# Performance work log

Hardware: AMD Instinct MI355X
Metric: run time of the kernel (lower is better)

## Reference

```python
import jax, jax.numpy as jnp
import numpy as np
import math

K_SLOTS = 64
DIM = 512
HEADS = 8
HEAD_DIM = DIM // HEADS
EPS = 1e-20
LN_EPS = 1e-5
SQRT_DIM = 1.0 / math.sqrt(HEAD_DIM)


def layernorm(x, g, b):
    mu = jnp.mean(x, axis=-1, keepdims=True)
    var = jnp.var(x, axis=-1, keepdims=True)
    return (x - mu) * jax.lax.rsqrt(var + LN_EPS) * g + b


def setup_inputs() -> dict:
    key = jax.random.key(0)
    ks = jax.random.split(key, 8)
    B, T = 8, 8192
    lim = 1.0 / math.sqrt(DIM)
    return {
        "X": jax.random.normal(ks[0], (B, T, DIM), jnp.float32),
        "slots_w": jax.random.normal(ks[1], (K_SLOTS, DIM), jnp.float32),
        "g_slots": jnp.ones((DIM,), jnp.float32),
        "b_slots": jnp.zeros((DIM,), jnp.float32),
        "Wk": jax.random.uniform(ks[2], (DIM, DIM), jnp.float32, -lim, lim),
        "bk": jax.random.uniform(ks[3], (DIM,), jnp.float32, -lim, lim),
        "Wv": jax.random.uniform(ks[4], (DIM, DIM), jnp.float32, -lim, lim),
        "bv": jax.random.uniform(ks[5], (DIM,), jnp.float32, -lim, lim),
        "g_after": jnp.ones((DIM,), jnp.float32),
        "b_after": jnp.zeros((DIM,), jnp.float32),
    }


def reference(X, slots_w, g_slots, b_slots, Wk, bk, Wv, bv, g_after, b_after):
    B, T, D = X.shape
    # slots -> queries, shared across batch: (K, D) -> (H, K, hd)
    S = layernorm(slots_w, g_slots, b_slots)
    Q = S.reshape(K_SLOTS, HEADS, HEAD_DIM).transpose(1, 0, 2)  # (H, K, hd)
    # key/value projections, head split: (B, T, D) -> (B, H, T, hd)
    Kx = (X @ Wk.T + bk).reshape(B, T, HEADS, HEAD_DIM).transpose(0, 2, 1, 3)
    V = (X @ Wv.T + bv).reshape(B, T, HEADS, HEAD_DIM).transpose(0, 2, 1, 3)
    # attention logits (B, H, K, T), scale = 1/sqrt(head_dim)
    A = jnp.einsum("hkd,bhsd->bhks", Q, Kx) * SQRT_DIM
    # softmax over the SLOT axis (k), then renormalize by row-sum over s
    W = jax.nn.softmax(A, axis=-2)
    C = jnp.sum(W, axis=-1, keepdims=True)  # (B, H, K, 1)
    A = W / (C + EPS)
    S_hat = jnp.einsum("bhks,bhsd->bhkd", A, V)  # (B, H, K, hd)
    S_hat = S_hat.transpose(0, 2, 1, 3).reshape(B, K_SLOTS, D)
    return layernorm(S_hat, g_after, b_after)
```

## Files before the change

### kernel.cpp

```cpp
#include <hip/hip_runtime.h>
#include <hip/hip_bf16.h>
#include <math.h>

typedef unsigned short ushort_t;
typedef unsigned int u32;

constexpr int D  = 512;
constexpr int T  = 8192;
constexpr int B  = 8;
constexpr int H  = 8;
constexpr int KS = 64;
constexpr int HD = 64;
constexpr float SCALE = 0.125f;
constexpr float LNEPS = 1e-5f;
constexpr float EPS   = 1e-20f;

constexpr int TC  = 128;
constexpr int CPB = 2;

constexpr size_t OFF_S    = 0;
constexpr size_t OFF_BQ   = 32768;
constexpr size_t OFF_SACC = 33280;
constexpr size_t OFF_CACC = 295424;
constexpr size_t OFF_WB2  = 299520;

typedef __attribute__((ext_vector_type(8))) short bf16x8;
typedef __attribute__((ext_vector_type(4))) float f32x4;
typedef __attribute__((ext_vector_type(4))) unsigned short us4;

typedef const __attribute__((address_space(1))) u32* gas_ptr;
typedef __attribute__((address_space(3))) u32* las_ptr;

__device__ __forceinline__ void gload16(const void* g, void* l) {
  __builtin_amdgcn_global_load_lds((gas_ptr)g, (las_ptr)l, 16, 0, 0);
}

__device__ __forceinline__ ushort_t f2bf(float x) {
  __hip_bfloat16 t = __float2bfloat16(x);
  return *(ushort_t*)&t;
}

__device__ __forceinline__ u32 pk2bf(float x, float y) {
  __hip_bfloat162 t = __float22bfloat162_rn(make_float2(x, y));
  return *(u32*)&t;
}

__device__ __forceinline__ bf16x8 cvt8(f32x4 a, f32x4 b) {
  union { bf16x8 v; u32 u[4]; } r;
  r.u[0] = pk2bf(a.x, a.y); r.u[1] = pk2bf(a.z, a.w);
  r.u[2] = pk2bf(b.x, b.y); r.u[3] = pk2bf(b.z, b.w);
  return r.v;
}

__global__ void ln_slots_kernel(const float* __restrict__ slots_w,
                                const float* __restrict__ g, const float* __restrict__ b,
                                float* __restrict__ S) {
  __shared__ float red[8];
  int k = blockIdx.x;
  int tid = threadIdx.x;
  float x0 = slots_w[k*D + tid];
  float x1 = slots_w[k*D + tid + 256];
  float s1 = x0 + x1, s2 = x0*x0 + x1*x1;
  for (int off = 32; off; off >>= 1) { s1 += __shfl_xor(s1, off); s2 += __shfl_xor(s2, off); }
  if ((tid & 63) == 0) { red[tid >> 6] = s1; red[4 + (tid >> 6)] = s2; }
  __syncthreads();
  s1 = red[0] + red[1] + red[2] + red[3];
  s2 = red[4] + red[5] + red[6] + red[7];
  float mu = s1 / D;
  float var = s2 / D - mu * mu;
  float rs = rsqrtf(var + LNEPS);
  S[k*D + tid]       = (x0 - mu) * rs * g[tid]       + b[tid];
  S[k*D + tid + 256] = (x1 - mu) * rs * g[tid + 256] + b[tid + 256];
}

__global__ void weff_kernel(const float* __restrict__ S, const float* __restrict__ Wk,
                            ushort_t* __restrict__ Wb2) {
  int gid = blockIdx.x * 256 + threadIdx.x;
  int in = gid & 511;
  int hk = gid >> 9;
  int h = hk >> 6, k = hk & 63;
  const float* srow = S + k*D + h*HD;
  const float* wcol = Wk + (size_t)(h*HD)*D + in;
  float acc = 0.f;
  #pragma unroll 8
  for (int d = 0; d < HD; ++d) acc += srow[d] * wcol[(size_t)d*D];
  Wb2[(size_t)(h*128 + k)*D + in] = f2bf(acc * SCALE);
}

__global__ void bq_kernel(const float* __restrict__ S, const float* __restrict__ bk,
                          float* __restrict__ bq) {
  int hk = blockIdx.x * 256 + threadIdx.x;
  int h = hk >> 6, k = hk & 63;
  float acc = 0.f;
  for (int d = 0; d < HD; ++d) acc += S[k*D + h*HD + d] * bk[h*HD + d];
  bq[hk] = acc * SCALE;
}

__global__ void wvcopy_kernel(const float* __restrict__ Wv, ushort_t* __restrict__ Wb2) {
  int gid = blockIdx.x * 256 + threadIdx.x;
  int in = gid & 511;
  int hd = gid >> 9;
  int h = hd >> 6, d = hd & 63;
  Wb2[(size_t)(h*128 + 64 + d)*D + in] = f2bf(Wv[(size_t)hd*D + in]);
}

__global__ void zero_kernel(float* __restrict__ p, int n) {
  int gid = blockIdx.x * 256 + threadIdx.x;
  if (gid < n) p[gid] = 0.f;
}

__global__ __launch_bounds__(256, 3) void main_kernel(
    const float* __restrict__ X, const ushort_t* __restrict__ Wb2,
    const float* __restrict__ bq, const float* __restrict__ bv,
    float* __restrict__ Sacc, float* __restrict__ Cacc) {
  __shared__ __align__(16) char smem[34816];
  float*    A_lds = (float*)smem;
  ushort_t* B_lds = (ushort_t*)(smem + 16384);
  ushort_t* W_lds = (ushort_t*)smem;
  ushort_t* V_lds = (ushort_t*)(smem + 17408);

  const int tid  = threadIdx.x;
  const int lane = tid & 63, w = tid >> 6;
  const int wm = w & 1, wn = w >> 1;
  const int m16 = lane & 15, q = lane >> 4;

  const int id = blockIdx.x;
  const int h  = (id >> 3) & 7;
  const int cg = (id & 7) | ((id >> 6) << 3);
  const int bh = (cg >> 5) * H + h;

  f32x4 acc2[4] = {};
  float csum[4] = {0.f, 0.f, 0.f, 0.f};

  for (int cc = 0; cc < CPB; ++cc) {
    const float* Xc = X + (size_t)(cg * CPB + cc) * TC * D;
    f32x4 acc[4][4] = {};

    for (int kb = 0; kb < D; kb += 32) {
      __syncthreads();
      #pragma unroll
      for (int m = 0; m < 4; ++m) {
        int li = tid + m * 256;
        int row = li >> 3, c = li & 7;
        gload16(Xc + (size_t)row * D + kb + c * 4, A_lds + (size_t)li * 4);
      }
      #pragma unroll
      for (int m = 0; m < 2; ++m) {
        int li = tid + m * 256;
        int col = li >> 2, c = li & 3;
        gload16(Wb2 + (size_t)(h * 128 + col) * D + kb + c * 8, B_lds + (size_t)li * 8);
      }
      __syncthreads();
      bf16x8 af[4], bf[4];
      #pragma unroll
      for (int i = 0; i < 4; ++i) {
        const f32x4* ap = (const f32x4*)(A_lds + (wm * 64 + i * 16 + m16) * 32 + q * 8);
        af[i] = cvt8(ap[0], ap[1]);
      }
      #pragma unroll
      for (int j = 0; j < 4; ++j)
        bf[j] = *(const bf16x8*)(B_lds + (wn * 64 + j * 16 + m16) * 32 + q * 8);
      #pragma unroll
      for (int i = 0; i < 4; ++i)
        #pragma unroll
        for (int j = 0; j < 4; ++j)
          acc[i][j] = __builtin_amdgcn_mfma_f32_16x16x32_bf16(af[i], bf[j], acc[i][j], 0, 0, 0);
    }
    __syncthreads();

    if (wn == 0) {
      float bqv[4];
      #pragma unroll
      for (int j = 0; j < 4; ++j) bqv[j] = bq[h * KS + j * 16 + m16];
      #pragma unroll
      for (int i = 0; i < 4; ++i) {
        us4 wp[4];
        #pragma unroll
        for (int r = 0; r < 4; ++r) {
          float v0 = acc[i][0][r] + bqv[0];
          float v1 = acc[i][1][r] + bqv[1];
          float v2 = acc[i][2][r] + bqv[2];
          float v3 = acc[i][3][r] + bqv[3];
          float mx = fmaxf(fmaxf(v0, v1), fmaxf(v2, v3));
          mx = fmaxf(mx, __shfl_xor(mx, 1));
          mx = fmaxf(mx, __shfl_xor(mx, 2));
          mx = fmaxf(mx, __shfl_xor(mx, 4));
          mx = fmaxf(mx, __shfl_xor(mx, 8));
          v0 = __expf(v0 - mx); v1 = __expf(v1 - mx);
          v2 = __expf(v2 - mx); v3 = __expf(v3 - mx);
          float s = v0 + v1 + v2 + v3;
          s += __shfl_xor(s, 1); s += __shfl_xor(s, 2);
          s += __shfl_xor(s, 4); s += __shfl_xor(s, 8);
          float inv = __builtin_amdgcn_rcpf(s);
          v0 *= inv; v1 *= inv; v2 *= inv; v3 *= inv;
          csum[0] += v0; csum[1] += v1; csum[2] += v2; csum[3] += v3;
          wp[0][r] = f2bf(v0); wp[1][r] = f2bf(v1);
          wp[2][r] = f2bf(v2); wp[3][r] = f2bf(v3);
        }
        #pragma unroll
        for (int j = 0; j < 4; ++j)
          *(us4*)(W_lds + (j * 16 + m16) * 136 + wm * 64 + i * 16 + q * 4) = wp[j];
      }
    } else {
      float bvv[4];
      #pragma unroll
      for (int j = 0; j < 4; ++j) bvv[j] = bv[h * HD + j * 16 + m16];
      #pragma unroll
      for (int i = 0; i < 4; ++i) {
        #pragma unroll
        for (int j = 0; j < 4; ++j) {
          us4 pk;
          pk.x = f2bf(acc[i][j][0] + bvv[j]);
          pk.y = f2bf(acc[i][j][1] + bvv[j]);
          pk.z = f2bf(acc[i][j][2] + bvv[j]);
          pk.w = f2bf(acc[i][j][3] + bvv[j]);
          *(us4*)(V_lds + (j * 16 + m16) * 136 + wm * 64 + i * 16 + q * 4) = pk;
        }
      }
    }
    __syncthreads();

    #pragma unroll
    for (int kk = 0; kk < 4; ++kk) {
      bf16x8 a = *(const bf16x8*)(W_lds + (w * 16 + m16) * 136 + kk * 32 + q * 8);
      #pragma unroll
      for (int j = 0; j < 4; ++j) {
        bf16x8 bb = *(const bf16x8*)(V_lds + (j * 16 + m16) * 136 + kk * 32 + q * 8);
        acc2[j] = __builtin_amdgcn_mfma_f32_16x16x32_bf16(a, bb, acc2[j], 0, 0, 0);
      }
    }
  }

  float* Sb = Sacc + (size_t)bh * KS * HD;
  #pragma unroll
  for (int j = 0; j < 4; ++j)
    #pragma unroll
    for (int r = 0; r < 4; ++r)
      atomicAdd(Sb + (w * 16 + q * 4 + r) * HD + j * 16 + m16, acc2[j][r]);

  if (wn == 0) {
    #pragma unroll
    for (int j = 0; j < 4; ++j) {
      float c = csum[j];
      c += __shfl_xor(c, 16);
      c += __shfl_xor(c, 32);
      if (q == 0) atomicAdd(Cacc + (size_t)bh * KS + j * 16 + m16, c);
    }
  }
}

__global__ void finalize_kernel(const float* __restrict__ Sacc, const float* __restrict__ Cacc,
                                const float* __restrict__ g, const float* __restrict__ bb,
                                float* __restrict__ out) {
  __shared__ float red[8];
  int bk_ = blockIdx.x;
  int b = bk_ >> 6, k = bk_ & 63;
  int tid = threadIdx.x;
  float v[2];
  #pragma unroll
  for (int m = 0; m < 2; ++m) {
    int d = tid + m*256;
    int h = d >> 6, dd = d & 63;
    float c = Cacc[((size_t)b*H + h)*KS + k];
    v[m] = Sacc[(((size_t)b*H + h)*KS + k)*HD + dd] / (c + EPS);
  }
  float s1 = v[0] + v[1], s2 = v[0]*v[0] + v[1]*v[1];
  for (int off = 32; off; off >>= 1) { s1 += __shfl_xor(s1, off); s2 += __shfl_xor(s2, off); }
  if ((tid & 63) == 0) { red[tid >> 6] = s1; red[4 + (tid >> 6)] = s2; }
  __syncthreads();
  s1 = red[0] + red[1] + red[2] + red[3];
  s2 = red[4] + red[5] + red[6] + red[7];
  float mu = s1 / D;
  float var = s2 / D - mu * mu;
  float rs = rsqrtf(var + LNEPS);
  #pragma unroll
  for (int m = 0; m < 2; ++m) {
    int d = tid + m*256;
    out[(size_t)bk_*D + d] = (v[m] - mu) * rs * g[d] + bb[d];
  }
}

extern "C" void kernel_launch(void* const* d_in, const int* in_sizes, int n_in,
                              void* d_out, int out_size, void* d_ws, size_t ws_size,
                              hipStream_t stream) {
  const float* X       = (const float*)d_in[0];
  const float* slots_w = (const float*)d_in[1];
  const float* g_slots = (const float*)d_in[2];
  const float* b_slots = (const float*)d_in[3];
  const float* Wk      = (const float*)d_in[4];
  const float* bk      = (const float*)d_in[5];
  const float* Wv      = (const float*)d_in[6];
  const float* bv      = (const float*)d_in[7];
  const float* g_after = (const float*)d_in[8];
  const float* b_after = (const float*)d_in[9];
  float* ws   = (float*)d_ws;
  float* S    = ws + OFF_S;
  float* bq   = ws + OFF_BQ;
  float* Sacc = ws + OFF_SACC;
  float* Cacc = ws + OFF_CACC;
  ushort_t* Wb2 = (ushort_t*)(ws + OFF_WB2);
  float* out  = (float*)d_out;

  hipLaunchKernelGGL(ln_slots_kernel, dim3(64), dim3(256), 0, stream, slots_w, g_slots, b_slots, S);
  hipLaunchKernelGGL(weff_kernel, dim3(1024), dim3(256), 0, stream, S, Wk, Wb2);
  hipLaunchKernelGGL(bq_kernel, dim3(2), dim3(256), 0, stream, S, bk, bq);
  hipLaunchKernelGGL(wvcopy_kernel, dim3(1024), dim3(256), 0, stream, Wv, Wb2);
  hipLaunchKernelGGL(zero_kernel, dim3(1040), dim3(256), 0, stream, Sacc, 266240);
  hipLaunchKernelGGL(main_kernel, dim3(2048), dim3(256), 0, stream, X, Wb2, bq, bv, Sacc, Cacc);
  hipLaunchKernelGGL(finalize_kernel, dim3(B * KS), dim3(256), 0, stream,
                     Sacc, Cacc, g_after, b_after, out);
}
```

Before: 362.6 us.

## Double-buffer LDS tiles in the projection GEMM and swizzle LDS layout

The K-loop of the fused key/value projection now double-buffers the X and weight tiles in LDS. The next 32-wide slice is issued with direct global-to-LDS loads before computing on the current one, and explicit vmcnt waits plus raw barriers replace the two __syncthreads per iteration. It also applies an XOR swizzle to the LDS layout to reduce bank conflicts on fragment reads. LDS use grows from 34 KB to 48 KB per block, which may lower occupancy below the 3-blocks launch bound, and a trailing sync is added after the slot GEMM.

```diff
diff --git a/kernel.cpp b/kernel.cpp
--- a/kernel.cpp
+++ b/kernel.cpp
@@ -113,9 +113,11 @@
     const float* __restrict__ X, const ushort_t* __restrict__ Wb2,
     const float* __restrict__ bq, const float* __restrict__ bv,
     float* __restrict__ Sacc, float* __restrict__ Cacc) {
-  __shared__ __align__(16) char smem[34816];
-  float*    A_lds = (float*)smem;
-  ushort_t* B_lds = (ushort_t*)(smem + 16384);
+  __shared__ __align__(16) char smem[49152];
+  float*    A0 = (float*)smem;
+  float*    A1 = (float*)(smem + 16384);
+  ushort_t* B0 = (ushort_t*)(smem + 32768);
+  ushort_t* B1 = (ushort_t*)(smem + 40960);
   ushort_t* W_lds = (ushort_t*)smem;
   ushort_t* V_lds = (ushort_t*)(smem + 17408);
 
@@ -129,6 +131,8 @@
   const int cg = (id & 7) | ((id >> 6) << 3);
   const int bh = (cg >> 5) * H + h;
 
+  const ushort_t* Wp = Wb2 + (size_t)h * 128 * D;
+
   f32x4 acc2[4] = {};
   float csum[4] = {0.f, 0.f, 0.f, 0.f};
 
@@ -136,35 +140,70 @@
     const float* Xc = X + (size_t)(cg * CPB + cc) * TC * D;
     f32x4 acc[4][4] = {};
 
-    for (int kb = 0; kb < D; kb += 32) {
-      __syncthreads();
-      #pragma unroll
-      for (int m = 0; m < 4; ++m) {
-        int li = tid + m * 256;
-        int row = li >> 3, c = li & 7;
-        gload16(Xc + (size_t)row * D + kb + c * 4, A_lds + (size_t)li * 4);
-      }
-      #pragma unroll
-      for (int m = 0; m < 2; ++m) {
-        int li = tid + m * 256;
-        int col = li >> 2, c = li & 3;
-        gload16(Wb2 + (size_t)(h * 128 + col) * D + kb + c * 8, B_lds + (size_t)li * 8);
-      }
-      __syncthreads();
-      bf16x8 af[4], bf[4];
+    #pragma unroll
+    for (int m = 0; m < 4; ++m) {
+      int li = tid + m * 256;
+      int row = li >> 3, c = li & 7;
+      gload16(Xc + (size_t)row * D + ((c ^ (row & 7)) * 4), A0 + (size_t)li * 4);
+    }
+    #pragma unroll
+    for (int m = 0; m < 2; ++m) {
+      int li = tid + m * 256;
+      int col = li >> 2, c = li & 3;
+      gload16(Wp + (size_t)col * D + ((c ^ ((col >> 1) & 3)) * 8), B0 + (size_t)li * 8);
+    }
+
+    #pragma unroll 2
+    for (int t = 0; t < 16; ++t) {
+      const float*    Ab = (t & 1) ? A1 : A0;
+      const ushort_t* Bb = (t & 1) ? B1 : B0;
+      if (t < 15) {
+        float*    An = (t & 1) ? A0 : A1;
+        ushort_t* Bn = (t & 1) ? B0 : B1;
+        int kb = (t + 1) * 32;
+        #pragma unroll
+        for (int m = 0; m < 4; ++m) {
+          int li = tid + m * 256;
+          int row = li >> 3, c = li & 7;
+          gload16(Xc + (size_t)row * D + kb + ((c ^ (row & 7)) * 4), An + (size_t)li * 4);
+        }
+        #pragma unroll
+        for (int m = 0; m < 2; ++m) {
+          int li = tid + m * 256;
+          int col = li >> 2, c = li & 3;
+          gload16(Wp + (size_t)col * D + kb + ((c ^ ((col >> 1) & 3)) * 8), Bn + (size_t)li * 8);
+        }
+        asm volatile("s_waitcnt vmcnt(6)" ::: "memory");
+      } else {
+        asm volatile("s_waitcnt vmcnt(0)" ::: "memory");
+      }
+      __builtin_amdgcn_s_barrier();
+      __builtin_amdgcn_sched_barrier(0);
+
+      bf16x8 af[4], bfr[4];
       #pragma unroll
       for (int i = 0; i < 4; ++i) {
-        const f32x4* ap = (const f32x4*)(A_lds + (wm * 64 + i * 16 + m16) * 32 + q * 8);
-        af[i] = cvt8(ap[0], ap[1]);
-      }
-      #pragma unroll
-      for (int j = 0; j < 4; ++j)
-        bf[j] = *(const bf16x8*)(B_lds + (wn * 64 + j * 16 + m16) * 32 + q * 8);
+        int r = wm * 64 + i * 16 + m16;
+        int sw = r & 7;
+        f32x4 a0 = *(const f32x4*)(Ab + (size_t)r * 32 + (((2 * q)     ^ sw) * 4));
+        f32x4 a1 = *(const f32x4*)(Ab + (size_t)r * 32 + (((2 * q + 1) ^ sw) * 4));
+        af[i] = cvt8(a0, a1);
+      }
+      #pragma unroll
+      for (int j = 0; j < 4; ++j) {
+        int cl = wn * 64 + j * 16 + m16;
+        bfr[j] = *(const bf16x8*)(Bb + (size_t)cl * 32 + ((q ^ ((cl >> 1) & 3)) * 8));
+      }
       #pragma unroll
       for (int i = 0; i < 4; ++i)
         #pragma unroll
         for (int j = 0; j < 4; ++j)
-          acc[i][j] = __builtin_amdgcn_mfma_f32_16x16x32_bf16(af[i], bf[j], acc[i][j], 0, 0, 0);
+          acc[i][j] = __builtin_amdgcn_mfma_f32_16x16x32_bf16(af[i], bfr[j], acc[i][j], 0, 0, 0);
+
+      if (t < 15) {
+        __builtin_amdgcn_sched_barrier(0);
+        __builtin_amdgcn_s_barrier();
+      }
     }
     __syncthreads();
 
@@ -229,6 +268,7 @@
         acc2[j] = __builtin_amdgcn_mfma_f32_16x16x32_bf16(a, bb, acc2[j], 0, 0, 0);
       }
     }
+    __syncthreads();
   }
 
   float* Sb = Sacc + (size_t)bh * KS * HD;
```

Measured after the change: 359.9 us. About the same (-0.7%).

## Load GEMM operands directly from global into registers with double buffering

Applied to the files above, without the earlier changes.

Replaces the LDS-staged global_load_lds tiling of the projection GEMM with per-lane direct global loads into registers, software-pipelined over two K-steps. This removes the two barriers per K-step and the LDS round trip. The cost is higher register use (launch bounds drop to 2 waves per SIMD) and loss of cross-wave operand sharing, since each X row is now fetched by both wn waves and each weight row by both wm waves. A barrier is added at the end of each chunk to protect the reused LDS buffers.

```diff
diff --git a/kernel.cpp b/kernel.cpp
--- a/kernel.cpp
+++ b/kernel.cpp
@@ -27,13 +27,6 @@
 typedef __attribute__((ext_vector_type(8))) short bf16x8;
 typedef __attribute__((ext_vector_type(4))) float f32x4;
 typedef __attribute__((ext_vector_type(4))) unsigned short us4;
-
-typedef const __attribute__((address_space(1))) u32* gas_ptr;
-typedef __attribute__((address_space(3))) u32* las_ptr;
-
-__device__ __forceinline__ void gload16(const void* g, void* l) {
-  __builtin_amdgcn_global_load_lds((gas_ptr)g, (las_ptr)l, 16, 0, 0);
-}
 
 __device__ __forceinline__ ushort_t f2bf(float x) {
   __hip_bfloat16 t = __float2bfloat16(x);
@@ -109,13 +102,11 @@
   if (gid < n) p[gid] = 0.f;
 }
 
-__global__ __launch_bounds__(256, 3) void main_kernel(
+__global__ __launch_bounds__(256, 2) void main_kernel(
     const float* __restrict__ X, const ushort_t* __restrict__ Wb2,
     const float* __restrict__ bq, const float* __restrict__ bv,
     float* __restrict__ Sacc, float* __restrict__ Cacc) {
   __shared__ __align__(16) char smem[34816];
-  float*    A_lds = (float*)smem;
-  ushort_t* B_lds = (ushort_t*)(smem + 16384);
   ushort_t* W_lds = (ushort_t*)smem;
   ushort_t* V_lds = (ushort_t*)(smem + 17408);
 
@@ -129,44 +120,78 @@
   const int cg = (id & 7) | ((id >> 6) << 3);
   const int bh = (cg >> 5) * H + h;
 
+  const ushort_t* bp[4];
+  #pragma unroll
+  for (int j = 0; j < 4; ++j)
+    bp[j] = Wb2 + (size_t)(h * 128 + wn * 64 + j * 16 + m16) * D + q * 8;
+
   f32x4 acc2[4] = {};
   float csum[4] = {0.f, 0.f, 0.f, 0.f};
 
   for (int cc = 0; cc < CPB; ++cc) {
     const float* Xc = X + (size_t)(cg * CPB + cc) * TC * D;
+    const float* ap[4];
+    #pragma unroll
+    for (int i = 0; i < 4; ++i)
+      ap[i] = Xc + (size_t)(wm * 64 + i * 16 + m16) * D + q * 8;
+
     f32x4 acc[4][4] = {};
 
-    for (int kb = 0; kb < D; kb += 32) {
-      __syncthreads();
-      #pragma unroll
-      for (int m = 0; m < 4; ++m) {
-        int li = tid + m * 256;
-        int row = li >> 3, c = li & 7;
-        gload16(Xc + (size_t)row * D + kb + c * 4, A_lds + (size_t)li * 4);
-      }
-      #pragma unroll
-      for (int m = 0; m < 2; ++m) {
-        int li = tid + m * 256;
-        int col = li >> 2, c = li & 3;
-        gload16(Wb2 + (size_t)(h * 128 + col) * D + kb + c * 8, B_lds + (size_t)li * 8);
-      }
-      __syncthreads();
-      bf16x8 af[4], bf[4];
+    f32x4 aL0[4], aH0[4], aL1[4], aH1[4];
+    bf16x8 bF0[4], bF1[4];
+
+    #pragma unroll
+    for (int i = 0; i < 4; ++i) {
+      aL0[i] = *(const f32x4*)(ap[i]);
+      aH0[i] = *(const f32x4*)(ap[i] + 4);
+    }
+    #pragma unroll
+    for (int j = 0; j < 4; ++j) bF0[j] = *(const bf16x8*)(bp[j]);
+
+    #pragma unroll
+    for (int tt = 0; tt < 8; ++tt) {
+      const int t1 = 2 * tt + 1;
       #pragma unroll
       for (int i = 0; i < 4; ++i) {
-        const f32x4* ap = (const f32x4*)(A_lds + (wm * 64 + i * 16 + m16) * 32 + q * 8);
-        af[i] = cvt8(ap[0], ap[1]);
-      }
-      #pragma unroll
-      for (int j = 0; j < 4; ++j)
-        bf[j] = *(const bf16x8*)(B_lds + (wn * 64 + j * 16 + m16) * 32 + q * 8);
-      #pragma unroll
-      for (int i = 0; i < 4; ++i)
-        #pragma unroll
-        for (int j = 0; j < 4; ++j)
-          acc[i][j] = __builtin_amdgcn_mfma_f32_16x16x32_bf16(af[i], bf[j], acc[i][j], 0, 0, 0);
-    }
-    __syncthreads();
+        aL1[i] = *(const f32x4*)(ap[i] + t1 * 32);
+        aH1[i] = *(const f32x4*)(ap[i] + t1 * 32 + 4);
+      }
+      #pragma unroll
+      for (int j = 0; j < 4; ++j) bF1[j] = *(const bf16x8*)(bp[j] + t1 * 32);
+
+      {
+        bf16x8 af[4];
+        #pragma unroll
+        for (int i = 0; i < 4; ++i) af[i] = cvt8(aL0[i], aH0[i]);
+        #pragma unroll
+        for (int i = 0; i < 4; ++i)
+          #pragma unroll
+          for (int j = 0; j < 4; ++j)
+            acc[i][j] = __builtin_amdgcn_mfma_f32_16x16x32_bf16(af[i], bF0[j], acc[i][j], 0, 0, 0);
+      }
+
+      if (tt < 7) {
+        const int t2 = 2 * tt + 2;
+        #pragma unroll
+        for (int i = 0; i < 4; ++i) {
+          aL0[i] = *(const f32x4*)(ap[i] + t2 * 32);
+          aH0[i] = *(const f32x4*)(ap[i] + t2 * 32 + 4);
+        }
+        #pragma unroll
+        for (int j = 0; j < 4; ++j) bF0[j] = *(const bf16x8*)(bp[j] + t2 * 32);
+      }
+
+      {
+        bf16x8 af[4];
+        #pragma unroll
+        for (int i = 0; i < 4; ++i) af[i] = cvt8(aL1[i], aH1[i]);
+        #pragma unroll
+        for (int i = 0; i < 4; ++i)
+          #pragma unroll
+          for (int j = 0; j < 4; ++j)
+            acc[i][j] = __builtin_amdgcn_mfma_f32_16x16x32_bf16(af[i], bF1[j], acc[i][j], 0, 0, 0);
+      }
+    }
 
     if (wn == 0) {
       float bqv[4];
@@ -229,6 +254,7 @@
         acc2[j] = __builtin_amdgcn_mfma_f32_16x16x32_bf16(a, bb, acc2[j], 0, 0, 0);
       }
     }
+    __syncthreads();
   }
 
   float* Sb = Sacc + (size_t)bh * KS * HD;
```

New measurement: 785.4 us. 2.17x slower.

## Double-buffer X tiles with swizzled LDS, load B directly, merge setup kernels

Applied to the files above, without the earlier changes.

The main GEMM loop now double-buffers the X tile in LDS, prefetching the next K-step with async loads while the current one computes. Manual vmcnt waits and barriers replace the two __syncthreads per step. The A tile uses an XOR swizzle to cut LDS bank conflicts, and the Wb2 fragments are read straight from global memory into registers rather than staged through LDS. The setup kernels (bq, weff, wvcopy, zero) are folded into ln_slots and one combined setup kernel to save launches, at the cost of more registers and tight asm ordering that may lower occupancy.

```diff
diff --git a/kernel.cpp b/kernel.cpp
--- a/kernel.cpp
+++ b/kernel.cpp
@@ -54,7 +54,8 @@
 
 __global__ void ln_slots_kernel(const float* __restrict__ slots_w,
                                 const float* __restrict__ g, const float* __restrict__ b,
-                                float* __restrict__ S) {
+                                const float* __restrict__ bk,
+                                float* __restrict__ S, float* __restrict__ bq) {
   __shared__ float red[8];
   int k = blockIdx.x;
   int tid = threadIdx.x;
@@ -69,44 +70,46 @@
   float mu = s1 / D;
   float var = s2 / D - mu * mu;
   float rs = rsqrtf(var + LNEPS);
-  S[k*D + tid]       = (x0 - mu) * rs * g[tid]       + b[tid];
-  S[k*D + tid + 256] = (x1 - mu) * rs * g[tid + 256] + b[tid + 256];
-}
-
-__global__ void weff_kernel(const float* __restrict__ S, const float* __restrict__ Wk,
-                            ushort_t* __restrict__ Wb2) {
-  int gid = blockIdx.x * 256 + threadIdx.x;
-  int in = gid & 511;
-  int hk = gid >> 9;
-  int h = hk >> 6, k = hk & 63;
-  const float* srow = S + k*D + h*HD;
-  const float* wcol = Wk + (size_t)(h*HD)*D + in;
-  float acc = 0.f;
-  #pragma unroll 8
-  for (int d = 0; d < HD; ++d) acc += srow[d] * wcol[(size_t)d*D];
-  Wb2[(size_t)(h*128 + k)*D + in] = f2bf(acc * SCALE);
-}
-
-__global__ void bq_kernel(const float* __restrict__ S, const float* __restrict__ bk,
-                          float* __restrict__ bq) {
-  int hk = blockIdx.x * 256 + threadIdx.x;
-  int h = hk >> 6, k = hk & 63;
-  float acc = 0.f;
-  for (int d = 0; d < HD; ++d) acc += S[k*D + h*HD + d] * bk[h*HD + d];
-  bq[hk] = acc * SCALE;
-}
-
-__global__ void wvcopy_kernel(const float* __restrict__ Wv, ushort_t* __restrict__ Wb2) {
-  int gid = blockIdx.x * 256 + threadIdx.x;
-  int in = gid & 511;
-  int hd = gid >> 9;
-  int h = hd >> 6, d = hd & 63;
-  Wb2[(size_t)(h*128 + 64 + d)*D + in] = f2bf(Wv[(size_t)hd*D + in]);
-}
-
-__global__ void zero_kernel(float* __restrict__ p, int n) {
-  int gid = blockIdx.x * 256 + threadIdx.x;
-  if (gid < n) p[gid] = 0.f;
+  float y0 = (x0 - mu) * rs * g[tid]       + b[tid];
+  float y1 = (x1 - mu) * rs * g[tid + 256] + b[tid + 256];
+  S[k*D + tid]       = y0;
+  S[k*D + tid + 256] = y1;
+  float p0 = y0 * bk[tid];
+  float p1 = y1 * bk[tid + 256];
+  for (int off = 32; off; off >>= 1) { p0 += __shfl_xor(p0, off); p1 += __shfl_xor(p1, off); }
+  if ((tid & 63) == 0) {
+    int w = tid >> 6;
+    bq[w * KS + k]       = p0 * SCALE;
+    bq[(4 + w) * KS + k] = p1 * SCALE;
+  }
+}
+
+__global__ void setup_kernel(const float* __restrict__ S, const float* __restrict__ Wk,
+                             const float* __restrict__ Wv,
+                             ushort_t* __restrict__ Wb2, float* __restrict__ Sacc) {
+  int id = blockIdx.x;
+  int tid = threadIdx.x;
+  if (id < 1024) {
+    int gid = id * 256 + tid;
+    int in = gid & 511;
+    int hk = gid >> 9;
+    int h = hk >> 6, k = hk & 63;
+    const float* srow = S + k*D + h*HD;
+    const float* wcol = Wk + (size_t)(h*HD)*D + in;
+    float acc = 0.f;
+    #pragma unroll 8
+    for (int d = 0; d < HD; ++d) acc += srow[d] * wcol[(size_t)d*D];
+    Wb2[(size_t)(h*128 + k)*D + in] = f2bf(acc * SCALE);
+  } else if (id < 2048) {
+    int gid = (id - 1024) * 256 + tid;
+    int in = gid & 511;
+    int hd = gid >> 9;
+    int h = hd >> 6, d = hd & 63;
+    Wb2[(size_t)(h*128 + 64 + d)*D + in] = f2bf(Wv[(size_t)hd*D + in]);
+  } else {
+    int gid = (id - 2048) * 256 + tid;
+    if (gid < 266240) Sacc[gid] = 0.f;
+  }
 }
 
 __global__ __launch_bounds__(256, 3) void main_kernel(
@@ -114,8 +117,8 @@
     const float* __restrict__ bq, const float* __restrict__ bv,
     float* __restrict__ Sacc, float* __restrict__ Cacc) {
   __shared__ __align__(16) char smem[34816];
-  float*    A_lds = (float*)smem;
-  ushort_t* B_lds = (ushort_t*)(smem + 16384);
+  float*    A0 = (float*)smem;
+  float*    A1 = (float*)(smem + 16384);
   ushort_t* W_lds = (ushort_t*)smem;
   ushort_t* V_lds = (ushort_t*)(smem + 17408);
 
@@ -129,43 +132,81 @@
   const int cg = (id & 7) | ((id >> 6) << 3);
   const int bh = (cg >> 5) * H + h;
 
+  const ushort_t* bp[4];
+  #pragma unroll
+  for (int j = 0; j < 4; ++j)
+    bp[j] = Wb2 + (size_t)(h * 128 + wn * 64 + j * 16 + m16) * D + q * 8;
+
   f32x4 acc2[4] = {};
   float csum[4] = {0.f, 0.f, 0.f, 0.f};
+
+#define STAGE_A(t, AB) do { \
+    _Pragma("unroll") \
+    for (int m_ = 0; m_ < 4; ++m_) { \
+      int li_ = tid + m_ * 256; \
+      int row_ = li_ >> 3, c_ = li_ & 7; \
+      gload16(Xc + (size_t)row_ * D + (t) * 32 + ((c_ ^ (row_ & 7)) * 4), \
+              (AB) + (size_t)li_ * 4); \
+    } \
+  } while (0)
+
+#define LOAD_B(t, reg) do { \
+    _Pragma("unroll") \
+    for (int j_ = 0; j_ < 4; ++j_) reg[j_] = *(const bf16x8*)(bp[j_] + (t) * 32); \
+  } while (0)
+
+#define COMPUTE(t, AB, BCUR) do { \
+    bf16x8 af_[4]; \
+    _Pragma("unroll") \
+    for (int i_ = 0; i_ < 4; ++i_) { \
+      int r_ = wm * 64 + i_ * 16 + m16; \
+      int sw_ = r_ & 7; \
+      f32x4 a0_ = *(const f32x4*)((AB) + (size_t)r_ * 32 + (((2 * q)     ^ sw_) * 4)); \
+      f32x4 a1_ = *(const f32x4*)((AB) + (size_t)r_ * 32 + (((2 * q + 1) ^ sw_) * 4)); \
+      af_[i_] = cvt8(a0_, a1_); \
+    } \
+    _Pragma("unroll") \
+    for (int i_ = 0; i_ < 4; ++i_) \
+      _Pragma("unroll") \
+      for (int j_ = 0; j_ < 4; ++j_) \
+        acc[i_][j_] = __builtin_amdgcn_mfma_f32_16x16x32_bf16(af_[i_], BCUR[j_], acc[i_][j_], 0, 0, 0); \
+  } while (0)
+
+#define STEP(t, AB, ABN, BCUR, BNXT) do { \
+    if ((t) < 15) { \
+      STAGE_A((t) + 1, ABN); \
+      LOAD_B((t) + 1, BNXT); \
+      asm volatile("s_waitcnt vmcnt(8)" ::: "memory"); \
+    } else { \
+      asm volatile("s_waitcnt vmcnt(0)" ::: "memory"); \
+    } \
+    __builtin_amdgcn_s_barrier(); \
+    __builtin_amdgcn_sched_barrier(0); \
+    COMPUTE(t, AB, BCUR); \
+    if ((t) < 15) { \
+      __builtin_amdgcn_sched_barrier(0); \
+      __builtin_amdgcn_s_barrier(); \
+    } \
+  } while (0)
 
   for (int cc = 0; cc < CPB; ++cc) {
     const float* Xc = X + (size_t)(cg * CPB + cc) * TC * D;
     f32x4 acc[4][4] = {};
-
-    for (int kb = 0; kb < D; kb += 32) {
-      __syncthreads();
-      #pragma unroll
-      for (int m = 0; m < 4; ++m) {
-        int li = tid + m * 256;
-        int row = li >> 3, c = li & 7;
-        gload16(Xc + (size_t)row * D + kb + c * 4, A_lds + (size_t)li * 4);
-      }
-      #pragma unroll
-      for (int m = 0; m < 2; ++m) {
-        int li = tid + m * 256;
-        int col = li >> 2, c = li & 3;
-        gload16(Wb2 + (size_t)(h * 128 + col) * D + kb + c * 8, B_lds + (size_t)li * 8);
-      }
-      __syncthreads();
-      bf16x8 af[4], bf[4];
-      #pragma unroll
-      for (int i = 0; i < 4; ++i) {
-        const f32x4* ap = (const f32x4*)(A_lds + (wm * 64 + i * 16 + m16) * 32 + q * 8);
-        af[i] = cvt8(ap[0], ap[1]);
-      }
-      #pragma unroll
-      for (int j = 0; j < 4; ++j)
-        bf[j] = *(const bf16x8*)(B_lds + (wn * 64 + j * 16 + m16) * 32 + q * 8);
-      #pragma unroll
-      for (int i = 0; i < 4; ++i)
-        #pragma unroll
-        for (int j = 0; j < 4; ++j)
-          acc[i][j] = __builtin_amdgcn_mfma_f32_16x16x32_bf16(af[i], bf[j], acc[i][j], 0, 0, 0);
-    }
+    bf16x8 bF0[4], bF1[4];
+
+    STAGE_A(0, A0);
+    LOAD_B(0, bF0);
+    __builtin_amdgcn_sched_barrier(0);
+
+    STEP( 0, A0, A1, bF0, bF1);  STEP( 1, A1, A0, bF1, bF0);
+    STEP( 2, A0, A1, bF0, bF1);  STEP( 3, A1, A0, bF1, bF0);
+    STEP( 4, A0, A1, bF0, bF1);  STEP( 5, A1, A0, bF1, bF0);
+    STEP( 6, A0, A1, bF0, bF1);  STEP( 7, A1, A0, bF1, bF0);
+    STEP( 8, A0, A1, bF0, bF1);  STEP( 9, A1, A0, bF1, bF0);
+    STEP(10, A0, A1, bF0, bF1);  STEP(11, A1, A0, bF1, bF0);
+    STEP(12, A0, A1, bF0, bF1);  STEP(13, A1, A0, bF1, bF0);
+    STEP(14, A0, A1, bF0, bF1);  STEP(15, A1, A0, bF1, bF0);
+
     __syncthreads();
 
     if (wn == 0) {
@@ -229,7 +270,13 @@
         acc2[j] = __builtin_amdgcn_mfma_f32_16x16x32_bf16(a, bb, acc2[j], 0, 0, 0);
       }
     }
-  }
+    __syncthreads();
+  }
+
+#undef STEP
+#undef COMPUTE
+#undef LOAD_B
+#undef STAGE_A
 
   float* Sb = Sacc + (size_t)bh * KS * HD;
   #pragma unroll
@@ -301,11 +348,9 @@
   ushort_t* Wb2 = (ushort_t*)(ws + OFF_WB2);
   float* out  = (float*)d_out;
 
-  hipLaunchKernelGGL(ln_slots_kernel, dim3(64), dim3(256), 0, stream, slots_w, g_slots, b_slots, S);
-  hipLaunchKernelGGL(weff_kernel, dim3(1024), dim3(256), 0, stream, S, Wk, Wb2);
-  hipLaunchKernelGGL(bq_kernel, dim3(2), dim3(256), 0, stream, S, bk, bq);
-  hipLaunchKernelGGL(wvcopy_kernel, dim3(1024), dim3(256), 0, stream, Wv, Wb2);
-  hipLaunchKernelGGL(zero_kernel, dim3(1040), dim3(256), 0, stream, Sacc, 266240);
+  hipLaunchKernelGGL(ln_slots_kernel, dim3(64), dim3(256), 0, stream,
+                     slots_w, g_slots, b_slots, bk, S, bq);
+  hipLaunchKernelGGL(setup_kernel, dim3(3088), dim3(256), 0, stream, S, Wk, Wv, Wb2, Sacc);
   hipLaunchKernelGGL(main_kernel, dim3(2048), dim3(256), 0, stream, X, Wb2, bq, bv, Sacc, Cacc);
   hipLaunchKernelGGL(finalize_kernel, dim3(B * KS), dim3(256), 0, stream,
                      Sacc, Cacc, g_after, b_after, out);
```

After: 429.0 us. 18.3% more time.
